# Performance work log

Hardware: AMD Instinct MI355X
Metric: run time of the kernel (lower is better)

Reference implementation:

```python
import jax, jax.numpy as jnp
import numpy as np

HEADS = 8
DIM_HEAD = 40
SCALE = DIM_HEAD ** -0.5


def setup_inputs() -> dict:
    key = jax.random.key(0)
    ks = jax.random.split(key, 6)
    B, S, D = 2, 4096, 320  # batch, seq (64x64 latent), query_dim
    inner = HEADS * DIM_HEAD  # 320
    s = 0.02
    return {
        "x": jax.random.normal(ks[0], (B, S, D), jnp.float32),
        "Wq": jax.random.normal(ks[1], (inner, D), jnp.float32) * s,
        "Wk": jax.random.normal(ks[2], (inner, D), jnp.float32) * s,
        "Wv": jax.random.normal(ks[3], (inner, D), jnp.float32) * s,
        "Wout": jax.random.normal(ks[4], (D, inner), jnp.float32) * s,
        "bout": jnp.zeros((D,), jnp.float32),
    }


def _split_heads(t):
    # [B, S, h*d] -> [B, h, S, d]
    B, S, _ = t.shape
    return t.reshape(B, S, HEADS, DIM_HEAD).transpose(0, 2, 1, 3)


def reference(x, Wq, Wk, Wv, Wout, bout):
    # self-attention path (context=None): k/v come from x
    q = _split_heads(x @ Wq.T)  # [B,h,S,d]
    k = _split_heads(x @ Wk.T)
    v = _split_heads(x @ Wv.T)
    # scores: materialized O(S^2) attention as in the torch einsum
    attn = jax.nn.softmax(jnp.einsum('bhid,bhjd->bhij', q, k) * SCALE, axis=-1)
    out = jnp.einsum('bhij,bhjd->bhid', attn, v)  # [B,h,S,d]
    B, _, S, _ = out.shape
    out = out.transpose(0, 2, 1, 3).reshape(B, S, HEADS * DIM_HEAD)
    return out @ Wout.T + bout  # to_out (dropout=0 -> identity)
```

## Files before the change

kernel.cpp:

```cpp
#include <hip/hip_runtime.h>

#define HEADS 8
#define DHEAD 40
#define SEQ   4096
#define BATCH 2
#define INNER 320
#define NBH   16
#define QSCALE ((float)(0.15811388300841897 * 1.4426950408889634))

typedef _Float16 f16;
typedef __attribute__((ext_vector_type(2)))  __fp16   fp16x2;
typedef __attribute__((ext_vector_type(4)))  _Float16 half4;
typedef __attribute__((ext_vector_type(8)))  _Float16 half8;
typedef __attribute__((ext_vector_type(16))) float    f32x16;

#if __has_builtin(__builtin_amdgcn_exp2f)
#define EXP2F(x) __builtin_amdgcn_exp2f(x)
#else
#define EXP2F(x) exp2f(x)
#endif

union H8 { half8 h8; fp16x2 p2[4]; uint4 u4; };

#define XN4   (BATCH * SEQ * INNER / 4)
#define WQKV4 (3 * INNER * INNER / 4)
#define WOUT4 (INNER * INNER / 4)
#define CONV_TOTAL (XN4 + WQKV4 + WOUT4)

__global__ __launch_bounds__(256)
void convert_kernel(const float* __restrict__ x,
                    const float* __restrict__ Wq,
                    const float* __restrict__ Wk,
                    const float* __restrict__ Wv,
                    const float* __restrict__ Wout,
                    f16* __restrict__ xh, f16* __restrict__ wh,
                    f16* __restrict__ wouth)
{
    int i = blockIdx.x * 256 + threadIdx.x;
    if (i >= CONV_TOTAL) return;
    float4 v;
    f16* dst;
    float sc = 1.0f;
    if (i < XN4) {
        v = ((const float4*)x)[i];
        dst = xh + 4 * (size_t)i;
    } else if (i < XN4 + WQKV4) {
        int j = i - XN4;
        if (j < 25600)      { v = ((const float4*)Wq)[j]; sc = QSCALE; }
        else if (j < 51200) { v = ((const float4*)Wk)[j - 25600]; }
        else                { v = ((const float4*)Wv)[j - 51200]; }
        dst = wh + 4 * (size_t)j;
    } else {
        int j = i - XN4 - WQKV4;
        v = ((const float4*)Wout)[j];
        dst = wouth + 4 * (size_t)j;
    }
    H8 u;
    u.p2[0] = __builtin_amdgcn_cvt_pkrtz(v.x * sc, v.y * sc);
    u.p2[1] = __builtin_amdgcn_cvt_pkrtz(v.z * sc, v.w * sc);
    *(uint2*)dst = make_uint2(u.u4.x, u.u4.y);
}

#define QSTR 72

__global__ __launch_bounds__(256)
void qkv_gemm_kernel(const f16* __restrict__ xh, const f16* __restrict__ wh,
                     f16* __restrict__ q, f16* __restrict__ k,
                     f16* __restrict__ vt)
{
    __shared__ f16 lds[(64 + 192) * QSTR];
    f16* As = lds;
    f16* Bs = lds + 64 * QSTR;

    const int tid = threadIdx.x;
    const int nb0 = blockIdx.x * 64;
    const int m0  = blockIdx.y * 64;
    const int wave = tid >> 6, lane = tid & 63, m = lane & 31, half = lane >> 5;
    const int mw = wave >> 1, nw = wave & 1;

    f32x16 acc[3];
    #pragma unroll
    for (int i = 0; i < 16; i++) { acc[0][i] = 0.f; acc[1][i] = 0.f; acc[2][i] = 0.f; }

    for (int k0 = 0; k0 < 320; k0 += 64) {
        __syncthreads();
        #pragma unroll
        for (int u = 0; u < 2; u++) {
            int idx = tid + 256 * u;
            int r = idx >> 3, c8 = idx & 7;
            *(uint4*)&As[r * QSTR + c8 * 8] =
                *(const uint4*)&xh[(size_t)(m0 + r) * 320 + k0 + c8 * 8];
        }
        #pragma unroll
        for (int u = 0; u < 6; u++) {
            int idx = tid + 256 * u;
            int r = idx >> 3, c8 = idx & 7;
            int wr = (r >> 6) * 320 + nb0 + (r & 63);
            *(uint4*)&Bs[r * QSTR + c8 * 8] =
                *(const uint4*)&wh[(size_t)wr * 320 + k0 + c8 * 8];
        }
        __syncthreads();
        #pragma unroll
        for (int c = 0; c < 4; c++) {
            half8 a = *(const half8*)&As[(mw * 32 + m) * QSTR + c * 16 + half * 8];
            #pragma unroll
            for (int t = 0; t < 3; t++) {
                half8 bf = *(const half8*)&Bs[(nw * 96 + t * 32 + m) * QSTR + c * 16 + half * 8];
                acc[t] = __builtin_amdgcn_mfma_f32_32x32x16_f16(a, bf, acc[t], 0, 0, 0);
            }
        }
    }

    const int b = m0 >> 12, s0 = m0 & 4095;

    #pragma unroll
    for (int t = 0; t < 3; t++) {
        int st = nw * 3 + t;
        if (st < 4) {
            f16* dst = (st < 2) ? q : k;
            int col = nb0 + (st & 1) * 32 + m;
            int h  = (col * 205) >> 13;
            int dd = col - h * 40;
            #pragma unroll
            for (int reg = 0; reg < 16; reg++) {
                int crow = 4 * half + (reg & 3) + 8 * (reg >> 2);
                int mg = m0 + mw * 32 + crow;
                int bb = mg >> 12, s = mg & 4095;
                dst[((size_t)(bb * 8 + h) * SEQ + s) * DHEAD + dd] = (f16)acc[t][reg];
            }
        }
    }

    __syncthreads();
    f16* Ct = lds;
    if (nw == 1) {
        #pragma unroll
        for (int t = 1; t < 3; t++) {
            int vr0 = (t - 1) * 32 + m;
            #pragma unroll
            for (int g = 0; g < 4; g++) {
                half4 hh;
                hh.x = (f16)acc[t][4 * g + 0]; hh.y = (f16)acc[t][4 * g + 1];
                hh.z = (f16)acc[t][4 * g + 2]; hh.w = (f16)acc[t][4 * g + 3];
                *(half4*)&Ct[vr0 * QSTR + mw * 32 + 8 * g + 4 * half] = hh;
            }
        }
    }
    __syncthreads();
    #pragma unroll
    for (int u = 0; u < 4; u++) {
        int idx = tid + 256 * u;
        int rl = idx >> 4, c4 = idx & 15;
        int col = nb0 + rl;
        int h  = (col * 205) >> 13;
        int dd = col - h * 40;
        int w4 = c4 & 3;
        int c4p = (c4 & ~3) | ((w4 == 1) ? 2 : (w4 == 2) ? 1 : w4);
        *(uint2*)&vt[((size_t)(b * 8 + h) * DHEAD + dd) * SEQ + s0 + c4p * 4] =
            *(const uint2*)&Ct[rl * QSTR + c4 * 4];
    }
}

#define KSTR 56
#define VSTR 72
#define LDS_K 0
#define LDS_V 3584
#define YN   (BATCH * SEQ * INNER)
#define LN   (NBH * SEQ)

__global__ __launch_bounds__(256, 4)
void attn_kernel(const f16* __restrict__ q, const f16* __restrict__ k,
                 const f16* __restrict__ vt,
                 f16* __restrict__ yp,
                 float* __restrict__ l32)
{
    __shared__ __align__(16) unsigned char ldsbuf[16896];
    f16*   ldsh = (f16*)ldsbuf;
    float* ldsf = (float*)ldsbuf;

    const int tid = threadIdx.x;
    const int blk = blockIdx.x;
    const int js = blk & 1;
    const int qt = (blk >> 1) & 63;
    const int bh = blk >> 7;
    const int b = bh >> 3, h = bh & 7;
    const int q0 = qt * 64;
    const int jbase = js * 2048;
    const int wave = tid >> 6, lane = tid & 63, m = lane & 31, half = lane >> 5;
    const int qs = wave >> 1, kh = wave & 1;

    if (tid < 128) {
        int key = tid >> 1, off = (tid & 1) * 4;
        *(uint2*)&ldsh[LDS_K + key * KSTR + 40 + off] = make_uint2(0u, 0u);
    }
    for (int i = tid; i < 24 * 16; i += 256) {
        int r = i >> 4, c = (i & 15) * 4;
        uint2 val = (r == 0) ? make_uint2(0x3C003C00u, 0x3C003C00u)
                             : make_uint2(0u, 0u);
        *(uint2*)&ldsh[LDS_V + (40 + r) * VSTR + c] = val;
    }

    half8 zero8;
    #pragma unroll
    for (int j = 0; j < 8; j++) zero8[j] = (f16)0.0f;
    half8 qa[3];
    {
        const f16* qb = q + ((size_t)bh * SEQ + q0 + qs * 32 + m) * DHEAD;
        qa[0] = *(const half8*)&qb[half * 8];
        qa[1] = *(const half8*)&qb[16 + half * 8];
        qa[2] = (half == 1) ? zero8 : *(const half8*)&qb[32];
    }

    f32x16 O[2];
    #pragma unroll
    for (int i = 0; i < 16; i++) { O[0][i] = 0.f; O[1][i] = 0.f; }

    const f16* kb = k  + (size_t)bh * SEQ * DHEAD;
    const f16* vb = vt + (size_t)bh * DHEAD * SEQ;

    const int krow0 = tid / 5,          kblk0 = tid % 5;
    const int krow1 = (256 + tid) / 5,  kblk1 = (256 + tid) % 5;
    const int vrow0 = tid >> 3,         vblk0 = tid & 7;
    const int vrow1 = (256 + tid) >> 3, vblk1 = (256 + tid) & 7;
    const bool lo64 = (tid < 64);

    uint4 ka0, ka1, va0, va1;
    ka0 = *(const uint4*)&kb[(size_t)(jbase + krow0) * DHEAD + kblk0 * 8];
    va0 = *(const uint4*)&vb[(size_t)vrow0 * SEQ + jbase + vblk0 * 8];
    if (lo64) {
        ka1 = *(const uint4*)&kb[(size_t)(jbase + krow1) * DHEAD + kblk1 * 8];
        va1 = *(const uint4*)&vb[(size_t)vrow1 * SEQ + jbase + vblk1 * 8];
    }

    for (int j0 = jbase; j0 < jbase + 2048; j0 += 64) {
        __syncthreads();
        *(uint4*)&ldsh[LDS_K + krow0 * KSTR + kblk0 * 8] = ka0;
        *(uint4*)&ldsh[LDS_V + vrow0 * VSTR + vblk0 * 8] = va0;
        if (lo64) {
            *(uint4*)&ldsh[LDS_K + krow1 * KSTR + kblk1 * 8] = ka1;
            *(uint4*)&ldsh[LDS_V + vrow1 * VSTR + vblk1 * 8] = va1;
        }
        __syncthreads();

        if (j0 + 64 < jbase + 2048) {
            const int jn = j0 + 64;
            ka0 = *(const uint4*)&kb[(size_t)(jn + krow0) * DHEAD + kblk0 * 8];
            va0 = *(const uint4*)&vb[(size_t)vrow0 * SEQ + jn + vblk0 * 8];
            if (lo64) {
                ka1 = *(const uint4*)&kb[(size_t)(jn + krow1) * DHEAD + kblk1 * 8];
                va1 = *(const uint4*)&vb[(size_t)vrow1 * SEQ + jn + vblk1 * 8];
            }
        }

        f32x16 S;
        #pragma unroll
        for (int i = 0; i < 16; i++) S[i] = 0.f;
        #pragma unroll
        for (int c = 0; c < 3; c++) {
            half8 kf = *(const half8*)&ldsh[LDS_K + (kh * 32 + m) * KSTR + c * 16 + half * 8];
            S = __builtin_amdgcn_mfma_f32_32x32x16_f16(kf, qa[c], S, 0, 0, 0);
        }

        H8 p0u, p1u;
        #pragma unroll
        for (int g = 0; g < 4; g++) {
            p0u.p2[g] = __builtin_amdgcn_cvt_pkrtz(EXP2F(S[2 * g]),     EXP2F(S[2 * g + 1]));
            p1u.p2[g] = __builtin_amdgcn_cvt_pkrtz(EXP2F(S[8 + 2 * g]), EXP2F(S[9 + 2 * g]));
        }

        #pragma unroll
        for (int c = 0; c < 2; c++) {
            half8 pc = c ? p1u.h8 : p0u.h8;
            half8 v0 = *(const half8*)&ldsh[LDS_V + m * VSTR + kh * 32 + c * 16 + half * 8];
            half8 v1 = *(const half8*)&ldsh[LDS_V + (32 + m) * VSTR + kh * 32 + c * 16 + half * 8];
            O[0] = __builtin_amdgcn_mfma_f32_32x32x16_f16(pc, v0, O[0], 0, 0, 0);
            O[1] = __builtin_amdgcn_mfma_f32_32x32x16_f16(pc, v1, O[1], 0, 0, 0);
        }
    }

    __syncthreads();
    if (kh == 1) {
        #pragma unroll
        for (int t = 0; t < 2; t++)
            #pragma unroll
            for (int reg = 0; reg < 16; reg++) {
                int row = 4 * half + (reg & 3) + 8 * (reg >> 2);
                ldsf[(qs * 32 + row) * 66 + t * 32 + m] = O[t][reg];
            }
    }
    __syncthreads();
    if (kh == 0) {
        f16* yb = yp + (size_t)js * YN
                + ((size_t)b * SEQ + q0 + qs * 32) * INNER + h * DHEAD;
        float* lb = l32 + (size_t)js * LN + ((size_t)bh << 12) + q0 + qs * 32;
        #pragma unroll
        for (int t = 0; t < 2; t++)
            #pragma unroll
            for (int reg = 0; reg < 16; reg++) {
                int row = 4 * half + (reg & 3) + 8 * (reg >> 2);
                O[t][reg] += ldsf[(qs * 32 + row) * 66 + t * 32 + m];
            }
        #pragma unroll
        for (int reg = 0; reg < 16; reg++) {
            int row = 4 * half + (reg & 3) + 8 * (reg >> 2);
            f16* yr = yb + (size_t)row * INNER;
            yr[m] = (f16)O[0][reg];
            if (m < 8) yr[32 + m] = (f16)O[1][reg];
            if (m == 8) lb[row] = O[1][reg];
        }
    }
}

#define ASTR 72

__global__ __launch_bounds__(256)
void out_proj_kernel(const f16* __restrict__ yp, const float* __restrict__ l32,
                     const f16* __restrict__ wouth,
                     const float* __restrict__ bout, float* __restrict__ out)
{
    __shared__ f16 lds[(128 + 64) * ASTR];
    f16* As = lds;
    f16* Bs = lds + 128 * ASTR;

    const int tid = threadIdx.x;
    const int m0 = blockIdx.y * 128;
    const int n0 = blockIdx.x * 64;
    const int wave = tid >> 6, lane = tid & 63, m = lane & 31, half = lane >> 5;

    f32x16 acc[2];
    #pragma unroll
    for (int i = 0; i < 16; i++) { acc[0][i] = 0.f; acc[1][i] = 0.f; }

    for (int k0 = 0; k0 < 320; k0 += 64) {
        __syncthreads();
        #pragma unroll
        for (int u = 0; u < 4; u++) {
            int idx = tid + 256 * u;
            int r = idx >> 3, c8 = idx & 7;
            int row = m0 + r;
            int bb = row >> 12, s = row & 4095;
            int col = k0 + c8 * 8;
            int h = (col * 205) >> 13;
            size_t off = (size_t)row * 320 + col;
            half8 a0 = *(const half8*)&yp[off];
            half8 a1 = *(const half8*)&yp[YN + off];
            float la = l32[(bb * 8 + h) * 4096 + s];
            float lb = l32[LN + (bb * 8 + h) * 4096 + s];
            float rinv = 1.0f / (la + lb);
            float f[8];
            #pragma unroll
            for (int e = 0; e < 8; e++)
                f[e] = ((float)a0[e] + (float)a1[e]) * rinv;
            H8 u8;
            u8.p2[0] = __builtin_amdgcn_cvt_pkrtz(f[0], f[1]);
            u8.p2[1] = __builtin_amdgcn_cvt_pkrtz(f[2], f[3]);
            u8.p2[2] = __builtin_amdgcn_cvt_pkrtz(f[4], f[5]);
            u8.p2[3] = __builtin_amdgcn_cvt_pkrtz(f[6], f[7]);
            *(uint4*)&As[r * ASTR + c8 * 8] = u8.u4;
        }
        #pragma unroll
        for (int u = 0; u < 2; u++) {
            int idx = tid + 256 * u;
            int r = idx >> 3, c8 = idx & 7;
            *(uint4*)&Bs[r * ASTR + c8 * 8] =
                *(const uint4*)&wouth[(size_t)(n0 + r) * 320 + k0 + c8 * 8];
        }
        __syncthreads();
        #pragma unroll
        for (int c = 0; c < 4; c++) {
            half8 a  = *(const half8*)&As[(wave * 32 + m) * ASTR + c * 16 + half * 8];
            half8 b0 = *(const half8*)&Bs[m * ASTR + c * 16 + half * 8];
            half8 b1 = *(const half8*)&Bs[(32 + m) * ASTR + c * 16 + half * 8];
            acc[0] = __builtin_amdgcn_mfma_f32_32x32x16_f16(a, b0, acc[0], 0, 0, 0);
            acc[1] = __builtin_amdgcn_mfma_f32_32x32x16_f16(a, b1, acc[1], 0, 0, 0);
        }
    }

    #pragma unroll
    for (int nt = 0; nt < 2; nt++) {
        int n = n0 + nt * 32 + m;
        float bias = bout[n];
        #pragma unroll
        for (int reg = 0; reg < 16; reg++) {
            int crow = 4 * half + (reg & 3) + 8 * (reg >> 2);
            out[(size_t)(m0 + wave * 32 + crow) * 320 + n] = acc[nt][reg] + bias;
        }
    }
}

extern "C" void kernel_launch(void* const* d_in, const int* in_sizes, int n_in,
                              void* d_out, int out_size, void* d_ws, size_t ws_size,
                              hipStream_t stream)
{
    const float* x    = (const float*)d_in[0];
    const float* Wq   = (const float*)d_in[1];
    const float* Wk   = (const float*)d_in[2];
    const float* Wv   = (const float*)d_in[3];
    const float* Wout = (const float*)d_in[4];
    const float* bout = (const float*)d_in[5];
    float* out = (float*)d_out;

    unsigned char* ws = (unsigned char*)d_ws;
    f16*   xh    = (f16*)(ws);
    f16*   wh    = (f16*)(ws +  5242880);
    f16*   wouth = (f16*)(ws +  5857280);
    f16*   qd    = (f16*)(ws +  6062080);
    f16*   kd    = (f16*)(ws + 11304960);
    f16*   vtd   = (f16*)(ws + 16547840);
    f16*   ypd   = (f16*)(ws + 21790720);
    float* l32   = (float*)(ws + 32276480);

    convert_kernel <<<2960,         256, 0, stream>>>(x, Wq, Wk, Wv, Wout, xh, wh, wouth);
    qkv_gemm_kernel<<<dim3(5, 128), 256, 0, stream>>>(xh, wh, qd, kd, vtd);
    attn_kernel    <<<2048,         256, 0, stream>>>(qd, kd, vtd, ypd, l32);
    out_proj_kernel<<<dim3(5, 64),  256, 0, stream>>>(ypd, l32, wouth, bout, out);
}
```

Before: 181.5 us.

## Double query rows per attention wave, write four partials, add combine kernel

Each attention block now covers 128 queries, and each wave handles 64 query rows against its half of the key tile. This reuses every K/V fragment loaded from LDS across two MFMA chains. The end-of-kernel LDS reduction between key-half waves is removed; each wave writes its own partial output and row sum, giving four partial buffers. A new combine kernel sums and normalizes them before the output projection. LDS strides are changed and occupancy is lowered to 3. The cost is more register pressure, extra global traffic for four partials, and an extra kernel launch.

```diff
diff --git a/kernel.cpp b/kernel.cpp
--- a/kernel.cpp
+++ b/kernel.cpp
@@ -161,161 +161,179 @@
     }
 }
 
-#define KSTR 56
-#define VSTR 72
+#define KSTR 58
+#define VSTR 66
 #define LDS_K 0
-#define LDS_V 3584
+#define LDS_V 3712
 #define YN   (BATCH * SEQ * INNER)
 #define LN   (NBH * SEQ)
 
-__global__ __launch_bounds__(256, 4)
+__global__ __launch_bounds__(256, 3)
 void attn_kernel(const f16* __restrict__ q, const f16* __restrict__ k,
                  const f16* __restrict__ vt,
                  f16* __restrict__ yp,
                  float* __restrict__ l32)
 {
-    __shared__ __align__(16) unsigned char ldsbuf[16896];
-    f16*   ldsh = (f16*)ldsbuf;
-    float* ldsf = (float*)ldsbuf;
+    __shared__ __align__(16) f16 ldsh[7936];
 
     const int tid = threadIdx.x;
     const int blk = blockIdx.x;
     const int js = blk & 1;
-    const int qt = (blk >> 1) & 63;
-    const int bh = blk >> 7;
+    const int qt = (blk >> 1) & 31;
+    const int bh = blk >> 6;
     const int b = bh >> 3, h = bh & 7;
-    const int q0 = qt * 64;
+    const int q0 = qt * 128;
     const int jbase = js * 2048;
     const int wave = tid >> 6, lane = tid & 63, m = lane & 31, half = lane >> 5;
-    const int qs = wave >> 1, kh = wave & 1;
-
-    if (tid < 128) {
-        int key = tid >> 1, off = (tid & 1) * 4;
-        *(uint2*)&ldsh[LDS_K + key * KSTR + 40 + off] = make_uint2(0u, 0u);
-    }
-    for (int i = tid; i < 24 * 16; i += 256) {
-        int r = i >> 4, c = (i & 15) * 4;
-        uint2 val = (r == 0) ? make_uint2(0x3C003C00u, 0x3C003C00u)
-                             : make_uint2(0u, 0u);
-        *(uint2*)&ldsh[LDS_V + (40 + r) * VSTR + c] = val;
+    const int qg = wave >> 1, kh = wave & 1;
+
+    if (tid < 64)
+        *(uint4*)&ldsh[LDS_K + tid * KSTR + 40] = make_uint4(0u, 0u, 0u, 0u);
+    for (int i = tid; i < 24 * VSTR; i += 256) {
+        int r = i / VSTR, c = i - r * VSTR;
+        ldsh[LDS_V + (40 + r) * VSTR + c] = (r == 0 && c < 64) ? (f16)1.0f : (f16)0.0f;
     }
 
     half8 zero8;
     #pragma unroll
     for (int j = 0; j < 8; j++) zero8[j] = (f16)0.0f;
-    half8 qa[3];
+    half8 qa[2][3];
     {
-        const f16* qb = q + ((size_t)bh * SEQ + q0 + qs * 32 + m) * DHEAD;
-        qa[0] = *(const half8*)&qb[half * 8];
-        qa[1] = *(const half8*)&qb[16 + half * 8];
-        qa[2] = (half == 1) ? zero8 : *(const half8*)&qb[32];
-    }
-
-    f32x16 O[2];
-    #pragma unroll
-    for (int i = 0; i < 16; i++) { O[0][i] = 0.f; O[1][i] = 0.f; }
+        const f16* qb = q + ((size_t)bh * SEQ + q0 + qg * 64 + m) * DHEAD;
+        #pragma unroll
+        for (int s = 0; s < 2; s++) {
+            qa[s][0] = *(const half8*)&qb[(size_t)s * 32 * DHEAD + half * 8];
+            qa[s][1] = *(const half8*)&qb[(size_t)s * 32 * DHEAD + 16 + half * 8];
+            qa[s][2] = (half == 1) ? zero8
+                     : *(const half8*)&qb[(size_t)s * 32 * DHEAD + 32];
+        }
+    }
+
+    f32x16 O00, O01, O10, O11;
+    #pragma unroll
+    for (int i = 0; i < 16; i++) { O00[i] = 0.f; O01[i] = 0.f; O10[i] = 0.f; O11[i] = 0.f; }
 
     const f16* kb = k  + (size_t)bh * SEQ * DHEAD;
     const f16* vb = vt + (size_t)bh * DHEAD * SEQ;
 
-    const int krow0 = tid / 5,          kblk0 = tid % 5;
-    const int krow1 = (256 + tid) / 5,  kblk1 = (256 + tid) % 5;
-    const int vrow0 = tid >> 3,         vblk0 = tid & 7;
-    const int vrow1 = (256 + tid) >> 3, vblk1 = (256 + tid) & 7;
+    const int kr0 = tid / 5,         kc0 = tid % 5;
+    const int kr1 = (256 + tid) / 5, kc1 = (256 + tid) % 5;
+    const int vr0 = tid >> 3,        vc0 = tid & 7;
+    const int vr1 = 32 + (tid >> 3);
     const bool lo64 = (tid < 64);
 
     uint4 ka0, ka1, va0, va1;
-    ka0 = *(const uint4*)&kb[(size_t)(jbase + krow0) * DHEAD + kblk0 * 8];
-    va0 = *(const uint4*)&vb[(size_t)vrow0 * SEQ + jbase + vblk0 * 8];
+    ka0 = *(const uint4*)&kb[(size_t)(jbase + kr0) * DHEAD + kc0 * 8];
+    va0 = *(const uint4*)&vb[(size_t)vr0 * SEQ + jbase + vc0 * 8];
     if (lo64) {
-        ka1 = *(const uint4*)&kb[(size_t)(jbase + krow1) * DHEAD + kblk1 * 8];
-        va1 = *(const uint4*)&vb[(size_t)vrow1 * SEQ + jbase + vblk1 * 8];
+        ka1 = *(const uint4*)&kb[(size_t)(jbase + kr1) * DHEAD + kc1 * 8];
+        va1 = *(const uint4*)&vb[(size_t)vr1 * SEQ + jbase + vc0 * 8];
     }
 
     for (int j0 = jbase; j0 < jbase + 2048; j0 += 64) {
         __syncthreads();
-        *(uint4*)&ldsh[LDS_K + krow0 * KSTR + kblk0 * 8] = ka0;
-        *(uint4*)&ldsh[LDS_V + vrow0 * VSTR + vblk0 * 8] = va0;
+        *(uint4*)&ldsh[LDS_K + kr0 * KSTR + kc0 * 8] = ka0;
+        *(uint4*)&ldsh[LDS_V + vr0 * VSTR + vc0 * 8] = va0;
         if (lo64) {
-            *(uint4*)&ldsh[LDS_K + krow1 * KSTR + kblk1 * 8] = ka1;
-            *(uint4*)&ldsh[LDS_V + vrow1 * VSTR + vblk1 * 8] = va1;
+            *(uint4*)&ldsh[LDS_K + kr1 * KSTR + kc1 * 8] = ka1;
+            *(uint4*)&ldsh[LDS_V + vr1 * VSTR + vc0 * 8] = va1;
         }
         __syncthreads();
 
         if (j0 + 64 < jbase + 2048) {
             const int jn = j0 + 64;
-            ka0 = *(const uint4*)&kb[(size_t)(jn + krow0) * DHEAD + kblk0 * 8];
-            va0 = *(const uint4*)&vb[(size_t)vrow0 * SEQ + jn + vblk0 * 8];
+            ka0 = *(const uint4*)&kb[(size_t)(jn + kr0) * DHEAD + kc0 * 8];
+            va0 = *(const uint4*)&vb[(size_t)vr0 * SEQ + jn + vc0 * 8];
             if (lo64) {
-                ka1 = *(const uint4*)&kb[(size_t)(jn + krow1) * DHEAD + kblk1 * 8];
-                va1 = *(const uint4*)&vb[(size_t)vrow1 * SEQ + jn + vblk1 * 8];
+                ka1 = *(const uint4*)&kb[(size_t)(jn + kr1) * DHEAD + kc1 * 8];
+                va1 = *(const uint4*)&vb[(size_t)vr1 * SEQ + jn + vc0 * 8];
             }
         }
 
-        f32x16 S;
-        #pragma unroll
-        for (int i = 0; i < 16; i++) S[i] = 0.f;
+        f32x16 S0, S1;
+        #pragma unroll
+        for (int i = 0; i < 16; i++) { S0[i] = 0.f; S1[i] = 0.f; }
         #pragma unroll
         for (int c = 0; c < 3; c++) {
             half8 kf = *(const half8*)&ldsh[LDS_K + (kh * 32 + m) * KSTR + c * 16 + half * 8];
-            S = __builtin_amdgcn_mfma_f32_32x32x16_f16(kf, qa[c], S, 0, 0, 0);
-        }
-
-        H8 p0u, p1u;
+            S0 = __builtin_amdgcn_mfma_f32_32x32x16_f16(kf, qa[0][c], S0, 0, 0, 0);
+            S1 = __builtin_amdgcn_mfma_f32_32x32x16_f16(kf, qa[1][c], S1, 0, 0, 0);
+        }
+
+        H8 p00, p01, p10, p11;
         #pragma unroll
         for (int g = 0; g < 4; g++) {
-            p0u.p2[g] = __builtin_amdgcn_cvt_pkrtz(EXP2F(S[2 * g]),     EXP2F(S[2 * g + 1]));
-            p1u.p2[g] = __builtin_amdgcn_cvt_pkrtz(EXP2F(S[8 + 2 * g]), EXP2F(S[9 + 2 * g]));
+            p00.p2[g] = __builtin_amdgcn_cvt_pkrtz(EXP2F(S0[2 * g]),     EXP2F(S0[2 * g + 1]));
+            p01.p2[g] = __builtin_amdgcn_cvt_pkrtz(EXP2F(S0[8 + 2 * g]), EXP2F(S0[9 + 2 * g]));
+            p10.p2[g] = __builtin_amdgcn_cvt_pkrtz(EXP2F(S1[2 * g]),     EXP2F(S1[2 * g + 1]));
+            p11.p2[g] = __builtin_amdgcn_cvt_pkrtz(EXP2F(S1[8 + 2 * g]), EXP2F(S1[9 + 2 * g]));
         }
 
         #pragma unroll
         for (int c = 0; c < 2; c++) {
-            half8 pc = c ? p1u.h8 : p0u.h8;
             half8 v0 = *(const half8*)&ldsh[LDS_V + m * VSTR + kh * 32 + c * 16 + half * 8];
             half8 v1 = *(const half8*)&ldsh[LDS_V + (32 + m) * VSTR + kh * 32 + c * 16 + half * 8];
-            O[0] = __builtin_amdgcn_mfma_f32_32x32x16_f16(pc, v0, O[0], 0, 0, 0);
-            O[1] = __builtin_amdgcn_mfma_f32_32x32x16_f16(pc, v1, O[1], 0, 0, 0);
-        }
-    }
-
-    __syncthreads();
-    if (kh == 1) {
-        #pragma unroll
-        for (int t = 0; t < 2; t++)
-            #pragma unroll
-            for (int reg = 0; reg < 16; reg++) {
-                int row = 4 * half + (reg & 3) + 8 * (reg >> 2);
-                ldsf[(qs * 32 + row) * 66 + t * 32 + m] = O[t][reg];
-            }
-    }
-    __syncthreads();
-    if (kh == 0) {
-        f16* yb = yp + (size_t)js * YN
-                + ((size_t)b * SEQ + q0 + qs * 32) * INNER + h * DHEAD;
-        float* lb = l32 + (size_t)js * LN + ((size_t)bh << 12) + q0 + qs * 32;
-        #pragma unroll
-        for (int t = 0; t < 2; t++)
-            #pragma unroll
-            for (int reg = 0; reg < 16; reg++) {
-                int row = 4 * half + (reg & 3) + 8 * (reg >> 2);
-                O[t][reg] += ldsf[(qs * 32 + row) * 66 + t * 32 + m];
-            }
+            half8 pa = c ? p01.h8 : p00.h8;
+            half8 pb = c ? p11.h8 : p10.h8;
+            O00 = __builtin_amdgcn_mfma_f32_32x32x16_f16(pa, v0, O00, 0, 0, 0);
+            O01 = __builtin_amdgcn_mfma_f32_32x32x16_f16(pa, v1, O01, 0, 0, 0);
+            O10 = __builtin_amdgcn_mfma_f32_32x32x16_f16(pb, v0, O10, 0, 0, 0);
+            O11 = __builtin_amdgcn_mfma_f32_32x32x16_f16(pb, v1, O11, 0, 0, 0);
+        }
+    }
+
+    const int ps = js * 2 + kh;
+    f16*   yb = yp  + (size_t)ps * YN + ((size_t)b * SEQ + q0 + qg * 64) * INNER + h * DHEAD;
+    float* lb = l32 + (size_t)ps * LN + ((size_t)bh << 12) + q0 + qg * 64;
+    #pragma unroll
+    for (int qsub = 0; qsub < 2; qsub++) {
+        const f32x16& Oa = qsub ? O10 : O00;
+        const f32x16& Ob = qsub ? O11 : O01;
         #pragma unroll
         for (int reg = 0; reg < 16; reg++) {
-            int row = 4 * half + (reg & 3) + 8 * (reg >> 2);
+            int row = qsub * 32 + 4 * half + (reg & 3) + 8 * (reg >> 2);
             f16* yr = yb + (size_t)row * INNER;
-            yr[m] = (f16)O[0][reg];
-            if (m < 8) yr[32 + m] = (f16)O[1][reg];
-            if (m == 8) lb[row] = O[1][reg];
-        }
-    }
+            yr[m] = (f16)Oa[reg];
+            if (m < 8) yr[32 + m] = (f16)Ob[reg];
+            if (m == 8) lb[row] = Ob[reg];
+        }
+    }
+}
+
+#define CGROUPS (BATCH * SEQ * INNER / 8)
+
+__global__ __launch_bounds__(256)
+void combine_kernel(const f16* __restrict__ yp, const float* __restrict__ l32,
+                    f16* __restrict__ yh)
+{
+    int i = blockIdx.x * 256 + threadIdx.x;
+    if (i >= CGROUPS) return;
+    int row = i / 40, grp = i - row * 40;
+    int b = row >> 12, s = row & 4095;
+    int h = grp / 5;
+    size_t off = (size_t)row * 320 + grp * 8;
+    half8 a0 = *(const half8*)&yp[off];
+    half8 a1 = *(const half8*)&yp[(size_t)YN + off];
+    half8 a2 = *(const half8*)&yp[2 * (size_t)YN + off];
+    half8 a3 = *(const half8*)&yp[3 * (size_t)YN + off];
+    int li = ((b * 8 + h) << 12) + s;
+    float rinv = 1.0f / (l32[li] + l32[LN + li] + l32[2 * LN + li] + l32[3 * LN + li]);
+    float f[8];
+    #pragma unroll
+    for (int e = 0; e < 8; e++)
+        f[e] = ((float)a0[e] + (float)a1[e] + (float)a2[e] + (float)a3[e]) * rinv;
+    H8 u8;
+    u8.p2[0] = __builtin_amdgcn_cvt_pkrtz(f[0], f[1]);
+    u8.p2[1] = __builtin_amdgcn_cvt_pkrtz(f[2], f[3]);
+    u8.p2[2] = __builtin_amdgcn_cvt_pkrtz(f[4], f[5]);
+    u8.p2[3] = __builtin_amdgcn_cvt_pkrtz(f[6], f[7]);
+    *(uint4*)&yh[off] = u8.u4;
 }
 
 #define ASTR 72
 
 __global__ __launch_bounds__(256)
-void out_proj_kernel(const f16* __restrict__ yp, const float* __restrict__ l32,
-                     const f16* __restrict__ wouth,
+void out_proj_kernel(const f16* __restrict__ yh, const f16* __restrict__ wouth,
                      const float* __restrict__ bout, float* __restrict__ out)
 {
     __shared__ f16 lds[(128 + 64) * ASTR];
@@ -337,26 +355,8 @@
         for (int u = 0; u < 4; u++) {
             int idx = tid + 256 * u;
             int r = idx >> 3, c8 = idx & 7;
-            int row = m0 + r;
-            int bb = row >> 12, s = row & 4095;
-            int col = k0 + c8 * 8;
-            int h = (col * 205) >> 13;
-            size_t off = (size_t)row * 320 + col;
-            half8 a0 = *(const half8*)&yp[off];
-            half8 a1 = *(const half8*)&yp[YN + off];
-            float la = l32[(bb * 8 + h) * 4096 + s];
-            float lb = l32[LN + (bb * 8 + h) * 4096 + s];
-            float rinv = 1.0f / (la + lb);
-            float f[8];
-            #pragma unroll
-            for (int e = 0; e < 8; e++)
-                f[e] = ((float)a0[e] + (float)a1[e]) * rinv;
-            H8 u8;
-            u8.p2[0] = __builtin_amdgcn_cvt_pkrtz(f[0], f[1]);
-            u8.p2[1] = __builtin_amdgcn_cvt_pkrtz(f[2], f[3]);
-            u8.p2[2] = __builtin_amdgcn_cvt_pkrtz(f[4], f[5]);
-            u8.p2[3] = __builtin_amdgcn_cvt_pkrtz(f[6], f[7]);
-            *(uint4*)&As[r * ASTR + c8 * 8] = u8.u4;
+            *(uint4*)&As[r * ASTR + c8 * 8] =
+                *(const uint4*)&yh[(size_t)(m0 + r) * 320 + k0 + c8 * 8];
         }
         #pragma unroll
         for (int u = 0; u < 2; u++) {
@@ -408,10 +408,12 @@
     f16*   kd    = (f16*)(ws + 11304960);
     f16*   vtd   = (f16*)(ws + 16547840);
     f16*   ypd   = (f16*)(ws + 21790720);
-    float* l32   = (float*)(ws + 32276480);
+    float* l32   = (float*)(ws + 42762240);
+    f16*   yhd   = (f16*)(ws + 43810816);
 
     convert_kernel <<<2960,         256, 0, stream>>>(x, Wq, Wk, Wv, Wout, xh, wh, wouth);
     qkv_gemm_kernel<<<dim3(5, 128), 256, 0, stream>>>(xh, wh, qd, kd, vtd);
-    attn_kernel    <<<2048,         256, 0, stream>>>(qd, kd, vtd, ypd, l32);
-    out_proj_kernel<<<dim3(5, 64),  256, 0, stream>>>(ypd, l32, wouth, bout, out);
-}
+    attn_kernel    <<<1024,         256, 0, stream>>>(qd, kd, vtd, ypd, l32);
+    combine_kernel <<<1280,         256, 0, stream>>>(ypd, l32, yhd);
+    out_proj_kernel<<<dim3(5, 64),  256, 0, stream>>>(yhd, wouth, bout, out);
+}
```

Measured after the change: 168.4 us. 1.08x faster.
